# Optimization experiments

Measured on AMD Instinct MI355X. Metric: run time of the kernel, lower is better.

## Reference

```python
import math
import jax, jax.numpy as jnp
import numpy as np

PROB_SPARSE_FACTOR = 0.4


def setup_inputs() -> dict:
    key = jax.random.key(0)
    kq, kk, kv = jax.random.split(key, 3)
    B, H, T, S, D = 2, 16, 2048, 2048, 64
    q = jax.random.normal(kq, (B, H, T, D), dtype=jnp.float32)
    k = jax.random.normal(kk, (B, H, S, D), dtype=jnp.float32)
    v = jax.random.normal(kv, (B, H, S, D), dtype=jnp.float32)
    return {"q": q, "k": k, "v": v}


def reference(q, k, v):
    B, H, T, D = q.shape
    S = k.shape[2]
    scaling = 1.0 / math.sqrt(D)
    # Informer-style top-u query count (static, derived from shapes)
    u = max(int(min(PROB_SPARSE_FACTOR * math.log(S), T * 0.5)), int(T * 0.3))

    # KLD scoring over full attention approximation: [B,H,T,S]
    attn_approx = jnp.einsum("bhtd,bhsd->bhts", q * scaling, k)
    attn_approx = jnp.clip(attn_approx, -50.0, 50.0)
    attn_approx = attn_approx - jnp.max(attn_approx, axis=-1, keepdims=True)
    sm = jax.nn.softmax(attn_approx, axis=-1)
    log_uniform = math.log(S)
    kl_score = jnp.sum(sm * (jnp.log(sm + 1e-10) + log_uniform), axis=-1)  # [B,H,T]

    # Select top-u most informative queries per (b,h)
    _, topk_idx = jax.lax.top_k(kl_score, u)  # [B,H,u]

    # Sparse attention only for selected queries
    q_red = jnp.take_along_axis(q, topk_idx[..., None], axis=2)  # [B,H,u,D]
    scores = jnp.einsum("bhud,bhsd->bhus", q_red, k) * scaling
    scores = jnp.clip(scores, -50.0, 50.0)
    scores = scores - jnp.max(scores, axis=-1, keepdims=True)
    w = jax.nn.softmax(scores, axis=-1)
    w = jnp.clip(w, 1e-9, 1.0)
    out_red = jnp.einsum("bhus,bhsd->bhud", w, v)  # [B,H,u,D]

    # Scatter reduced outputs back into a zero-initialized full output
    b_i = jnp.arange(B)[:, None, None]
    h_i = jnp.arange(H)[None, :, None]
    out = jnp.zeros_like(q).at[b_i, h_i, topk_idx].set(out_red)
    return out
```

## Files before the change

### kernel.cpp

```cpp
#include <hip/hip_runtime.h>
#include <math.h>

#define T_DIM 2048
#define S_DIM 2048
#define D_DIM 64
#define BH_DIM 32
#define U_SEL 614
#define QROWS 80
#define LOG_S_D 7.624618986159398
#define LOG2E_F 1.4426950408889634f
#define LN2_D 0.6931471805599453
#define SCL_Q (0.125f * LOG2E_F)

typedef __attribute__((ext_vector_type(8))) short bf16x8;
typedef __attribute__((ext_vector_type(4))) short bf16x4;
typedef __attribute__((ext_vector_type(4))) float f32x4;

__device__ __forceinline__ unsigned short bf16_rne(float x) {
  unsigned u = __float_as_uint(x);
  u += 0x7FFF + ((u >> 16) & 1);
  return (unsigned short)(u >> 16);
}
__device__ __forceinline__ float bf16_to_f(unsigned short h) {
  return __uint_as_float(((unsigned)h) << 16);
}

#define GLD_LDS16(g, l)                                                        \
  __builtin_amdgcn_global_load_lds(                                            \
      (const __attribute__((address_space(1))) unsigned int*)(const void*)(g), \
      (__attribute__((address_space(3))) unsigned int*)(void*)(l), 16, 0, 0)

__device__ __forceinline__ void stage_img16(const unsigned short* __restrict__ g,
                                            unsigned short* l, int lane, int w) {
#pragma unroll
  for (int it = 0; it < 4; ++it) {
    const int chunk = it * 4 + w;
    GLD_LDS16((const char*)g + chunk * 1024 + lane * 16, (char*)l + chunk * 1024);
  }
}
__device__ __forceinline__ void stage_img8(const unsigned short* __restrict__ g,
                                           unsigned short* l, int lane, int w) {
#pragma unroll
  for (int it = 0; it < 2; ++it) {
    const int chunk = it * 4 + w;
    GLD_LDS16((const char*)g + chunk * 1024 + lane * 16, (char*)l + chunk * 1024);
  }
}

__device__ __forceinline__ bf16x8 ldfrag_sw(const unsigned short* buf, int row, int chunk) {
  return *(const bf16x8*)(buf + (row << 6) + (((chunk) ^ (row & 7)) << 3));
}
__device__ __forceinline__ bf16x8 ldfrag_k128(const unsigned short* buf, int row, int chunk) {
  return *(const bf16x8*)(buf + ((row >> 6) << 12) + ((row & 63) << 6) +
                          (((chunk) ^ (row & 7)) << 3));
}

__global__ __launch_bounds__(256) void convert_kernel(
    const float* __restrict__ kin, const float* __restrict__ vin,
    unsigned short* __restrict__ kimg, unsigned short* __restrict__ vt_g,
    float* __restrict__ out) {
  __shared__ float vld[128][65];
  const int jb = blockIdx.x;
  const int tid = threadIdx.x;
  if (jb < 1024) {
    const int bh = jb >> 5, tl = jb & 31;
    const float* src = kin + ((size_t)bh * 2048 + tl * 64) * 64;
    unsigned short* dst = kimg + (size_t)(bh * 32 + tl) * 8192;
#pragma unroll
    for (int g = 0; g < 2; ++g) {
      const int flat = g * 256 + tid;
      const int r = flat >> 3, c = flat & 7;
      const float4 f0 = *(const float4*)(src + r * 64 + c * 8);
      const float4 f1 = *(const float4*)(src + r * 64 + c * 8 + 4);
      const float xs[8] = {f0.x, f0.y, f0.z, f0.w, f1.x, f1.y, f1.z, f1.w};
      bf16x8 hv, lv;
#pragma unroll
      for (int j = 0; j < 8; ++j) {
        const unsigned short h = bf16_rne(xs[j]);
        hv[j] = (short)h;
        lv[j] = (short)bf16_rne(xs[j] - bf16_to_f(h));
      }
      const int base = (r << 6) + ((c ^ (r & 7)) << 3);
      *(bf16x8*)(dst + base) = hv;
      *(bf16x8*)(dst + 4096 + base) = lv;
    }
  } else if (jb < 1536) {
    const int jv = jb - 1024;
    const int bh = jv >> 4, tl = jv & 15;
    const float* src = vin + ((size_t)bh * 2048 + tl * 128) * 64;
#pragma unroll
    for (int g = 0; g < 8; ++g) {
      const int f = g * 256 + tid;
      const int r = f >> 4, c4 = f & 15;
      const float4 x = *(const float4*)(src + r * 64 + c4 * 4);
      vld[r][c4 * 4 + 0] = x.x;
      vld[r][c4 * 4 + 1] = x.y;
      vld[r][c4 * 4 + 2] = x.z;
      vld[r][c4 * 4 + 3] = x.w;
    }
    __syncthreads();
    unsigned short* dst = vt_g + (size_t)(bh * 16 + tl) * 8192;
#pragma unroll
    for (int g = 0; g < 4; ++g) {
      const int oc = g * 256 + tid;
      const int d = oc >> 4, cc = oc & 15;
      bf16x8 hv;
#pragma unroll
      for (int j = 0; j < 8; ++j) hv[j] = (short)bf16_rne(vld[cc * 8 + j][d]);
      *(bf16x8*)(dst + (d << 7) + (((cc ^ (d & 15))) << 3)) = hv;
    }
  } else {
    float4* o4 = (float4*)out;
    const size_t b = (size_t)(jb - 1536);
#pragma unroll
    for (int g = 0; g < 8; ++g)
      o4[b * 2048 + g * 256 + tid] = make_float4(0.f, 0.f, 0.f, 0.f);
  }
}

__global__ __launch_bounds__(256, 4) void kl_score_mfma(
    const float* __restrict__ q, const unsigned short* __restrict__ kimg,
    float2* __restrict__ zw) {
  __shared__ __align__(16) unsigned short lbuf[2][8192];
  const int b = blockIdx.x;
  const int bh = b & 31;
  const int t0 = ((b >> 5) & 15) * 128;
  const int shalf = b >> 9;
  const int tid = threadIdx.x;
  const int lane = tid & 63, w = tid >> 6, quad = lane >> 4, l15 = lane & 15;
  const float* qb = q + (size_t)bh * (2048 * 64) + (size_t)t0 * 64;
  const unsigned short* kb = kimg + (size_t)bh * (32 * 8192);
  const int tg0 = shalf * 16;

  {
#pragma unroll
    for (int g = 0; g < 4; ++g) {
      const int flat = g * 256 + tid;
      const int r = flat >> 3, c = flat & 7;
      const float4 f0 = *(const float4*)(qb + r * 64 + c * 8);
      const float4 f1 = *(const float4*)(qb + r * 64 + c * 8 + 4);
      const float xs[8] = {f0.x, f0.y, f0.z, f0.w, f1.x, f1.y, f1.z, f1.w};
      bf16x8 hv, lv;
#pragma unroll
      for (int j = 0; j < 8; ++j) {
        const float x = xs[j] * SCL_Q;
        const unsigned short h = bf16_rne(x);
        hv[j] = (short)h;
        lv[j] = (short)bf16_rne(x - bf16_to_f(h));
      }
      const int r2 = r & 63, hi2 = r >> 6;
      const int base = hi2 * 4096 + (r2 << 6) + ((c ^ (r2 & 7)) << 3);
      *(bf16x8*)(&lbuf[0][0] + base) = hv;
      *(bf16x8*)(&lbuf[1][0] + base) = lv;
    }
  }
  __syncthreads();

  bf16x8 ah[2][2], al[2][2];
#pragma unroll
  for (int rt = 0; rt < 2; ++rt) {
    const int row = w * 32 + rt * 16 + l15;
#pragma unroll
    for (int kc = 0; kc < 2; ++kc) {
      ah[rt][kc] = ldfrag_k128(&lbuf[0][0], row, kc * 4 + quad);
      al[rt][kc] = ldfrag_k128(&lbuf[1][0], row, kc * 4 + quad);
    }
  }
  __syncthreads();

  stage_img16(kb + (size_t)tg0 * 8192, &lbuf[0][0], lane, w);
  __syncthreads();

  float Zf[8], Wf[8];
#pragma unroll
  for (int i = 0; i < 8; ++i) { Zf[i] = 0.f; Wf[i] = 0.f; }

  for (int t = 0; t < 16; ++t) {
    if (t < 15)
      stage_img16(kb + (size_t)(tg0 + t + 1) * 8192, &lbuf[(t + 1) & 1][0], lane, w);
    const unsigned short* cb = &lbuf[t & 1][0];

    f32x4 acc[2][4];
#pragma unroll
    for (int rt = 0; rt < 2; ++rt)
#pragma unroll
      for (int ct = 0; ct < 4; ++ct) acc[rt][ct] = (f32x4){0.f, 0.f, 0.f, 0.f};

#pragma unroll
    for (int ct = 0; ct < 4; ++ct) {
      const int srow = ct * 16 + l15;
      const bf16x8 bh0 = ldfrag_sw(cb, srow, quad);
      const bf16x8 bl0 = ldfrag_sw(cb + 4096, srow, quad);
      const bf16x8 bh1 = ldfrag_sw(cb, srow, 4 + quad);
      const bf16x8 bl1 = ldfrag_sw(cb + 4096, srow, 4 + quad);
#pragma unroll
      for (int rt = 0; rt < 2; ++rt) {
        f32x4 c = acc[rt][ct];
        c = __builtin_amdgcn_mfma_f32_16x16x32_bf16(ah[rt][0], bh0, c, 0, 0, 0);
        c = __builtin_amdgcn_mfma_f32_16x16x32_bf16(al[rt][0], bh0, c, 0, 0, 0);
        c = __builtin_amdgcn_mfma_f32_16x16x32_bf16(ah[rt][0], bl0, c, 0, 0, 0);
        c = __builtin_amdgcn_mfma_f32_16x16x32_bf16(ah[rt][1], bh1, c, 0, 0, 0);
        c = __builtin_amdgcn_mfma_f32_16x16x32_bf16(al[rt][1], bh1, c, 0, 0, 0);
        c = __builtin_amdgcn_mfma_f32_16x16x32_bf16(ah[rt][1], bl1, c, 0, 0, 0);
        acc[rt][ct] = c;
      }
    }

#pragma unroll
    for (int rt = 0; rt < 2; ++rt)
#pragma unroll
      for (int r = 0; r < 4; ++r) {
        float zp = 0.f, wp = 0.f;
#pragma unroll
        for (int ct = 0; ct < 4; ++ct) {
          const float tt = acc[rt][ct][r];
          const float e = exp2f(tt);
          zp += e;
          wp = fmaf(e, tt, wp);
        }
        Zf[rt * 4 + r] += zp;
        Wf[rt * 4 + r] += wp;
      }
    __syncthreads();
  }

#pragma unroll
  for (int i = 0; i < 8; ++i) {
    float Zt = Zf[i], Wt = Wf[i];
#pragma unroll
    for (int mask = 1; mask <= 8; mask <<= 1) {
      Zt += __shfl_xor(Zt, mask);
      Wt += __shfl_xor(Wt, mask);
    }
    if (l15 == 0) {
      const int row = t0 + w * 32 + (i >> 2) * 16 + quad * 4 + (i & 3);
      zw[((size_t)shalf * 32 + bh) * 2048 + row] = make_float2(Zt, Wt);
    }
  }
}

__global__ __launch_bounds__(1024) void topk_kernel(const float2* __restrict__ zw,
                                                    int* __restrict__ topk) {
  __shared__ float sv[2048];
  __shared__ int si[2048];
  const int bh = blockIdx.x;
  const int tid = threadIdx.x;
  for (int i = tid; i < 2048; i += 1024) {
    const float2 a = zw[(size_t)bh * 2048 + i];
    const float2 c = zw[(size_t)(32 + bh) * 2048 + i];
    const double Z = (double)a.x + (double)c.x;
    const double W = (double)a.y + (double)c.y;
    sv[i] = (float)(LN2_D * (W / Z) - log(Z) + LOG_S_D);
    si[i] = i;
  }
  __syncthreads();
  for (int kk = 2; kk <= 2048; kk <<= 1) {
    for (int j = kk >> 1; j > 0; j >>= 1) {
      const int p = tid;
      const int i = ((p & ~(j - 1)) << 1) | (p & (j - 1));
      const int pr = i | j;
      const float v1 = sv[i], v2 = sv[pr];
      const int i1 = si[i], i2 = si[pr];
      const bool beforePI = (v2 > v1) || (v2 == v1 && i2 < i1);
      const bool dirDesc = ((i & kk) == 0);
      const bool doSwap = dirDesc ? beforePI : !beforePI;
      if (doSwap) { sv[i] = v2; sv[pr] = v1; si[i] = i2; si[pr] = i1; }
      __syncthreads();
    }
  }
  for (int i = tid; i < U_SEL; i += 1024) topk[bh * U_SEL + i] = si[i];
}

struct __align__(16) SmC {
  union { unsigned short kt[2][8192]; float obuf[QROWS * 64]; } a;
  union { unsigned short vt[2][8192]; float zred[4][QROWS]; } b;
  unsigned short qs[QROWS * 64];
  unsigned short ps[4][QROWS * 40];
};

__global__ __launch_bounds__(256, 1) void sparse_attn_mfma(
    const float* __restrict__ q, const unsigned short* __restrict__ kimg,
    const unsigned short* __restrict__ vt_g, const int* __restrict__ topk,
    float* __restrict__ out) {
  __shared__ SmC sm;
  const int b = blockIdx.x;
  const int bh = b & 31;
  const int l0 = (b >> 5) * QROWS;
  const int tid = threadIdx.x;
  const int lane = tid & 63, w = tid >> 6, quad = lane >> 4, l15 = lane & 15;
  const float* qb = q + (size_t)bh * (2048 * 64);
  const unsigned short* kb = kimg + (size_t)bh * (32 * 8192);
  const unsigned short* vtb = vt_g + (size_t)bh * (16 * 8192);
  const int* tkb = topk + bh * U_SEL;

  {
#pragma unroll
    for (int g = 0; g < 3; ++g) {
      const int ch = g * 256 + tid;
      if (ch < QROWS * 8) {
        const int r = ch >> 3, c = ch & 7;
        const int l = l0 + r;
        const int row = (l < U_SEL) ? tkb[l] : tkb[0];
        const float4 f0 = *(const float4*)(qb + (size_t)row * 64 + c * 8);
        const float4 f1 = *(const float4*)(qb + (size_t)row * 64 + c * 8 + 4);
        const float xs[8] = {f0.x, f0.y, f0.z, f0.w, f1.x, f1.y, f1.z, f1.w};
        bf16x8 hv;
#pragma unroll
        for (int j = 0; j < 8; ++j) hv[j] = (short)bf16_rne(xs[j] * SCL_Q);
        *(bf16x8*)&sm.qs[(r << 6) + ((c ^ (r & 7)) << 3)] = hv;
      }
    }
  }
  stage_img8(kb, sm.a.kt[0], lane, w);
  stage_img8(kb + 8192, sm.a.kt[0] + 4096, lane, w);
  stage_img16(vtb, sm.b.vt[0], lane, w);
  __syncthreads();

  bf16x8 qf[5][2];
#pragma unroll
  for (int nt = 0; nt < 5; ++nt)
#pragma unroll
    for (int kc = 0; kc < 2; ++kc)
      qf[nt][kc] = ldfrag_sw(sm.qs, nt * 16 + l15, kc * 4 + quad);

  float zrun[5] = {0.f, 0.f, 0.f, 0.f, 0.f};
  f32x4 oacc[5][4];
#pragma unroll
  for (int a = 0; a < 5; ++a)
#pragma unroll
    for (int b2 = 0; b2 < 4; ++b2) oacc[a][b2] = (f32x4){0.f, 0.f, 0.f, 0.f};

  for (int st = 0; st < 16; ++st) {
    if (st < 15) {
      unsigned short* kd = sm.a.kt[(st + 1) & 1];
      unsigned short* vd = sm.b.vt[(st + 1) & 1];
      stage_img8(kb + (size_t)(2 * st + 2) * 8192, kd, lane, w);
      stage_img8(kb + (size_t)(2 * st + 3) * 8192, kd + 4096, lane, w);
      stage_img16(vtb + (size_t)(st + 1) * 8192, vd, lane, w);
    }
    const unsigned short* kcur = sm.a.kt[st & 1];
    const unsigned short* vcur = sm.b.vt[st & 1];

    const int ar0 = w * 32 + l15, ar1 = w * 32 + 16 + l15;
    const bf16x8 a00 = ldfrag_k128(kcur, ar0, quad);
    const bf16x8 a01 = ldfrag_k128(kcur, ar0, 4 + quad);
    const bf16x8 a10 = ldfrag_k128(kcur, ar1, quad);
    const bf16x8 a11 = ldfrag_k128(kcur, ar1, 4 + quad);

    f32x4 sacc[2][5];
    __builtin_amdgcn_s_setprio(1);
#pragma unroll
    for (int mt = 0; mt < 2; ++mt)
#pragma unroll
      for (int nt = 0; nt < 5; ++nt) {
        f32x4 c = (f32x4){0.f, 0.f, 0.f, 0.f};
        c = __builtin_amdgcn_mfma_f32_16x16x32_bf16(mt ? a10 : a00, qf[nt][0], c, 0, 0, 0);
        c = __builtin_amdgcn_mfma_f32_16x16x32_bf16(mt ? a11 : a01, qf[nt][1], c, 0, 0, 0);
        sacc[mt][nt] = c;
      }
    __builtin_amdgcn_s_setprio(0);

#pragma unroll
    for (int nt = 0; nt < 5; ++nt) {
      float zl = 0.f;
#pragma unroll
      for (int mt = 0; mt < 2; ++mt) {
        bf16x4 pw;
#pragma unroll
        for (int r = 0; r < 4; ++r) {
          const float p = exp2f(sacc[mt][nt][r]);
          zl += p;
          pw[r] = (short)bf16_rne(p);
        }
        *(bf16x4*)&sm.ps[w][(nt * 16 + l15) * 40 + mt * 16 + quad * 4] = pw;
      }
      zrun[nt] += zl;
    }

    bf16x8 vbf[4];
#pragma unroll
    for (int dt = 0; dt < 4; ++dt) {
      const int d = dt * 16 + l15;
      vbf[dt] = *(const bf16x8*)&vcur[(d << 7) + (((w * 4 + quad) ^ l15) << 3)];
    }

    __builtin_amdgcn_s_setprio(1);
#pragma unroll
    for (int mtq = 0; mtq < 5; ++mtq) {
      const bf16x8 pa = *(const bf16x8*)&sm.ps[w][(mtq * 16 + l15) * 40 + quad * 8];
#pragma unroll
      for (int dt = 0; dt < 4; ++dt)
        oacc[mtq][dt] = __builtin_amdgcn_mfma_f32_16x16x32_bf16(pa, vbf[dt], oacc[mtq][dt], 0, 0, 0);
    }
    __builtin_amdgcn_s_setprio(0);
    __syncthreads();
  }

#pragma unroll
  for (int nt = 0; nt < 5; ++nt) {
    float z = zrun[nt];
    z += __shfl_xor(z, 16);
    z += __shfl_xor(z, 32);
    if (quad == 0) sm.b.zred[w][nt * 16 + l15] = z;
  }
  for (int i = tid; i < QROWS * 64; i += 256) sm.a.obuf[i] = 0.f;
  __syncthreads();
#pragma unroll
  for (int mtq = 0; mtq < 5; ++mtq)
#pragma unroll
    for (int r = 0; r < 4; ++r) {
      const int qr = mtq * 16 + quad * 4 + r;
#pragma unroll
      for (int dt = 0; dt < 4; ++dt)
        atomicAdd(&sm.a.obuf[qr * 64 + dt * 16 + l15], oacc[mtq][dt][r]);
    }
  __syncthreads();
  {
#pragma unroll
    for (int it = 0; it < 2; ++it) {
      const int tt = it * 256 + tid;
      if (tt < QROWS * 4) {
        const int qr = tt >> 2, seg = tt & 3;
        const int l = l0 + qr;
        if (l < U_SEL) {
          const float Zt = sm.b.zred[0][qr] + sm.b.zred[1][qr] +
                           sm.b.zred[2][qr] + sm.b.zred[3][qr];
          const float inv = 1.0f / Zt;
          const int row = tkb[l];
          float* op = &out[((size_t)bh * T_DIM + row) * 64 + seg * 16];
          const float* ob = &sm.a.obuf[qr * 64 + seg * 16];
#pragma unroll
          for (int j = 0; j < 4; ++j) {
            float4 o;
            o.x = ob[j * 4 + 0] * inv;
            o.y = ob[j * 4 + 1] * inv;
            o.z = ob[j * 4 + 2] * inv;
            o.w = ob[j * 4 + 3] * inv;
            *(float4*)&op[j * 4] = o;
          }
        }
      }
    }
  }
}

extern "C" void kernel_launch(void* const* d_in, const int* in_sizes, int n_in,
                              void* d_out, int out_size, void* d_ws, size_t ws_size,
                              hipStream_t stream) {
  const float* q = (const float*)d_in[0];
  const float* k = (const float*)d_in[1];
  const float* v = (const float*)d_in[2];
  float* out = (float*)d_out;
  char* ws = (char*)d_ws;
  float2* zw = (float2*)ws;
  int* topk = (int*)(ws + 1048576);
  unsigned short* kimg = (unsigned short*)(ws + 1310720);
  unsigned short* vt_g = (unsigned short*)(ws + 18087936);

  convert_kernel<<<dim3(2048), dim3(256), 0, stream>>>(k, v, kimg, vt_g, out);
  kl_score_mfma<<<dim3(1024), dim3(256), 0, stream>>>(q, kimg, zw);
  topk_kernel<<<dim3(BH_DIM), dim3(1024), 0, stream>>>(zw, topk);
  sparse_attn_mfma<<<dim3(256), dim3(256), 0, stream>>>(q, kimg, vt_g, topk, out);
}
```

Before: 231.2 us.

## Precompute split-bf16 Q image, split KL scoring over four S chunks, use hardware exp2

Q scaling and hi/lo bf16 splitting move into the convert kernel, writing a swizzled Q image that kl_score loads directly into LDS with async global-to-LDS copies. The KL scoring grid doubles by splitting the key dimension into four quarters instead of two, and topk sums four partial Z/W pairs. exp2f is replaced with the raw v_exp_f32 hardware instruction in both scoring and sparse attention. This trades extra global writes and reads of the Q image and a larger workspace for more parallelism and a cheaper exponential. The hardware exp also drops denormal handling.

```diff
diff --git a/kernel.cpp b/kernel.cpp
--- a/kernel.cpp
+++ b/kernel.cpp
@@ -24,6 +24,15 @@
 __device__ __forceinline__ float bf16_to_f(unsigned short h) {
   return __uint_as_float(((unsigned)h) << 16);
 }
+__device__ __forceinline__ float exp2_hw(float x) {
+#if __has_builtin(__builtin_amdgcn_exp2f)
+  return __builtin_amdgcn_exp2f(x);
+#else
+  float r;
+  asm("v_exp_f32 %0, %1" : "=v"(r) : "v"(x));
+  return r;
+#endif
+}
 
 #define GLD_LDS16(g, l)                                                        \
   __builtin_amdgcn_global_load_lds(                                            \
@@ -57,15 +66,19 @@
 
 __global__ __launch_bounds__(256) void convert_kernel(
     const float* __restrict__ kin, const float* __restrict__ vin,
-    unsigned short* __restrict__ kimg, unsigned short* __restrict__ vt_g,
+    const float* __restrict__ qin, unsigned short* __restrict__ kimg,
+    unsigned short* __restrict__ vt_g, unsigned short* __restrict__ qimg,
     float* __restrict__ out) {
   __shared__ float vld[128][65];
   const int jb = blockIdx.x;
   const int tid = threadIdx.x;
-  if (jb < 1024) {
-    const int bh = jb >> 5, tl = jb & 31;
-    const float* src = kin + ((size_t)bh * 2048 + tl * 64) * 64;
-    unsigned short* dst = kimg + (size_t)(bh * 32 + tl) * 8192;
+  if (jb < 2048) {
+    const bool isq = jb >= 1024;
+    const int jj = jb & 1023;
+    const int bh = jj >> 5, tl = jj & 31;
+    const float* src = (isq ? qin : kin) + ((size_t)bh * 2048 + tl * 64) * 64;
+    unsigned short* dst = (isq ? qimg : kimg) + (size_t)(bh * 32 + tl) * 8192;
+    const float scl = isq ? SCL_Q : 1.0f;
 #pragma unroll
     for (int g = 0; g < 2; ++g) {
       const int flat = g * 256 + tid;
@@ -76,16 +89,17 @@
       bf16x8 hv, lv;
 #pragma unroll
       for (int j = 0; j < 8; ++j) {
-        const unsigned short h = bf16_rne(xs[j]);
+        const float x = xs[j] * scl;
+        const unsigned short h = bf16_rne(x);
         hv[j] = (short)h;
-        lv[j] = (short)bf16_rne(xs[j] - bf16_to_f(h));
+        lv[j] = (short)bf16_rne(x - bf16_to_f(h));
       }
       const int base = (r << 6) + ((c ^ (r & 7)) << 3);
       *(bf16x8*)(dst + base) = hv;
       *(bf16x8*)(dst + 4096 + base) = lv;
     }
-  } else if (jb < 1536) {
-    const int jv = jb - 1024;
+  } else if (jb < 2560) {
+    const int jv = jb - 2048;
     const int bh = jv >> 4, tl = jv & 15;
     const float* src = vin + ((size_t)bh * 2048 + tl * 128) * 64;
 #pragma unroll
@@ -111,7 +125,7 @@
     }
   } else {
     float4* o4 = (float4*)out;
-    const size_t b = (size_t)(jb - 1536);
+    const size_t b = (size_t)(jb - 2560);
 #pragma unroll
     for (int g = 0; g < 8; ++g)
       o4[b * 2048 + g * 256 + tid] = make_float4(0.f, 0.f, 0.f, 0.f);
@@ -119,51 +133,34 @@
 }
 
 __global__ __launch_bounds__(256, 4) void kl_score_mfma(
-    const float* __restrict__ q, const unsigned short* __restrict__ kimg,
+    const unsigned short* __restrict__ qimg, const unsigned short* __restrict__ kimg,
     float2* __restrict__ zw) {
   __shared__ __align__(16) unsigned short lbuf[2][8192];
   const int b = blockIdx.x;
   const int bh = b & 31;
-  const int t0 = ((b >> 5) & 15) * 128;
-  const int shalf = b >> 9;
+  const int tt = (b >> 5) & 15;
+  const int sq = b >> 9;
   const int tid = threadIdx.x;
   const int lane = tid & 63, w = tid >> 6, quad = lane >> 4, l15 = lane & 15;
-  const float* qb = q + (size_t)bh * (2048 * 64) + (size_t)t0 * 64;
+  const unsigned short* qb = qimg + (size_t)(bh * 32 + tt * 2) * 8192;
   const unsigned short* kb = kimg + (size_t)bh * (32 * 8192);
-  const int tg0 = shalf * 16;
-
-  {
-#pragma unroll
-    for (int g = 0; g < 4; ++g) {
-      const int flat = g * 256 + tid;
-      const int r = flat >> 3, c = flat & 7;
-      const float4 f0 = *(const float4*)(qb + r * 64 + c * 8);
-      const float4 f1 = *(const float4*)(qb + r * 64 + c * 8 + 4);
-      const float xs[8] = {f0.x, f0.y, f0.z, f0.w, f1.x, f1.y, f1.z, f1.w};
-      bf16x8 hv, lv;
-#pragma unroll
-      for (int j = 0; j < 8; ++j) {
-        const float x = xs[j] * SCL_Q;
-        const unsigned short h = bf16_rne(x);
-        hv[j] = (short)h;
-        lv[j] = (short)bf16_rne(x - bf16_to_f(h));
-      }
-      const int r2 = r & 63, hi2 = r >> 6;
-      const int base = hi2 * 4096 + (r2 << 6) + ((c ^ (r2 & 7)) << 3);
-      *(bf16x8*)(&lbuf[0][0] + base) = hv;
-      *(bf16x8*)(&lbuf[1][0] + base) = lv;
-    }
-  }
-  __syncthreads();
-
+  const int tg0 = sq * 8;
+
+  stage_img16(qb, &lbuf[0][0], lane, w);
+  stage_img16(qb + 8192, &lbuf[1][0], lane, w);
+  __syncthreads();
+
+  const unsigned short* lb = &lbuf[0][0];
   bf16x8 ah[2][2], al[2][2];
 #pragma unroll
   for (int rt = 0; rt < 2; ++rt) {
     const int row = w * 32 + rt * 16 + l15;
+    const int tile = row >> 6, r64 = row & 63;
 #pragma unroll
     for (int kc = 0; kc < 2; ++kc) {
-      ah[rt][kc] = ldfrag_k128(&lbuf[0][0], row, kc * 4 + quad);
-      al[rt][kc] = ldfrag_k128(&lbuf[1][0], row, kc * 4 + quad);
+      const int off = tile * 8192 + (r64 << 6) + (((kc * 4 + quad) ^ (r64 & 7)) << 3);
+      ah[rt][kc] = *(const bf16x8*)(lb + off);
+      al[rt][kc] = *(const bf16x8*)(lb + 4096 + off);
     }
   }
   __syncthreads();
@@ -175,8 +172,8 @@
 #pragma unroll
   for (int i = 0; i < 8; ++i) { Zf[i] = 0.f; Wf[i] = 0.f; }
 
-  for (int t = 0; t < 16; ++t) {
-    if (t < 15)
+  for (int t = 0; t < 8; ++t) {
+    if (t < 7)
       stage_img16(kb + (size_t)(tg0 + t + 1) * 8192, &lbuf[(t + 1) & 1][0], lane, w);
     const unsigned short* cb = &lbuf[t & 1][0];
 
@@ -213,10 +210,10 @@
         float zp = 0.f, wp = 0.f;
 #pragma unroll
         for (int ct = 0; ct < 4; ++ct) {
-          const float tt = acc[rt][ct][r];
-          const float e = exp2f(tt);
+          const float tv = acc[rt][ct][r];
+          const float e = exp2_hw(tv);
           zp += e;
-          wp = fmaf(e, tt, wp);
+          wp = fmaf(e, tv, wp);
         }
         Zf[rt * 4 + r] += zp;
         Wf[rt * 4 + r] += wp;
@@ -233,8 +230,8 @@
       Wt += __shfl_xor(Wt, mask);
     }
     if (l15 == 0) {
-      const int row = t0 + w * 32 + (i >> 2) * 16 + quad * 4 + (i & 3);
-      zw[((size_t)shalf * 32 + bh) * 2048 + row] = make_float2(Zt, Wt);
+      const int row = tt * 128 + w * 32 + (i >> 2) * 16 + quad * 4 + (i & 3);
+      zw[((size_t)sq * 32 + bh) * 2048 + row] = make_float2(Zt, Wt);
     }
   }
 }
@@ -246,10 +243,13 @@
   const int bh = blockIdx.x;
   const int tid = threadIdx.x;
   for (int i = tid; i < 2048; i += 1024) {
-    const float2 a = zw[(size_t)bh * 2048 + i];
-    const float2 c = zw[(size_t)(32 + bh) * 2048 + i];
-    const double Z = (double)a.x + (double)c.x;
-    const double W = (double)a.y + (double)c.y;
+    double Z = 0.0, W = 0.0;
+#pragma unroll
+    for (int sq = 0; sq < 4; ++sq) {
+      const float2 a = zw[((size_t)sq * 32 + bh) * 2048 + i];
+      Z += (double)a.x;
+      W += (double)a.y;
+    }
     sv[i] = (float)(LN2_D * (W / Z) - log(Z) + LOG_S_D);
     si[i] = i;
   }
@@ -368,7 +368,7 @@
         bf16x4 pw;
 #pragma unroll
         for (int r = 0; r < 4; ++r) {
-          const float p = exp2f(sacc[mt][nt][r]);
+          const float p = exp2_hw(sacc[mt][nt][r]);
           zl += p;
           pw[r] = (short)bf16_rne(p);
         }
@@ -453,12 +453,13 @@
   float* out = (float*)d_out;
   char* ws = (char*)d_ws;
   float2* zw = (float2*)ws;
-  int* topk = (int*)(ws + 1048576);
-  unsigned short* kimg = (unsigned short*)(ws + 1310720);
-  unsigned short* vt_g = (unsigned short*)(ws + 18087936);
-
-  convert_kernel<<<dim3(2048), dim3(256), 0, stream>>>(k, v, kimg, vt_g, out);
-  kl_score_mfma<<<dim3(1024), dim3(256), 0, stream>>>(q, kimg, zw);
+  int* topk = (int*)(ws + 2097152);
+  unsigned short* kimg = (unsigned short*)(ws + 2179072);
+  unsigned short* vt_g = (unsigned short*)(ws + 18956288);
+  unsigned short* qimg = (unsigned short*)(ws + 27344896);
+
+  convert_kernel<<<dim3(3072), dim3(256), 0, stream>>>(k, v, q, kimg, vt_g, qimg, out);
+  kl_score_mfma<<<dim3(2048), dim3(256), 0, stream>>>(qimg, kimg, zw);
   topk_kernel<<<dim3(BH_DIM), dim3(1024), 0, stream>>>(zw, topk);
   sparse_attn_mfma<<<dim3(256), dim3(256), 0, stream>>>(q, kimg, vt_g, topk, out);
 }
```

Result: slower. 653.2 us (+182.5%).
